# Optimization experiments

Measured on AMD Instinct MI355X. Metric: run time of the kernel, lower is better.

Reference implementation:

```python
import jax, jax.numpy as jnp
import numpy as np

N, D, d = 4_000_000, 3, 2

def setup_inputs() -> dict:
    key = jax.random.key(0)
    k1, k2, k3 = jax.random.split(key, 3)
    points = jax.random.normal(k1, (N, D), dtype=jnp.float32)
    reconstructed_points = jax.random.normal(k2, (N, D), dtype=jnp.float32)
    orthonormal_frame = jax.random.normal(k3, (N, D, d), dtype=jnp.float32)
    return {"points": points, "reconstructed_points": reconstructed_points,
            "orthonormal_frame": orthonormal_frame}

def reference(points, reconstructed_points, orthonormal_frame):
    # r: [N, D] residual
    r = reconstructed_points - points
    # project r onto the tangent frame: y = H @ (H^T r), H: [N, D, d]
    coeffs = jnp.einsum('nij,ni->nj', orthonormal_frame, r)   # [N, d]
    y = jnp.einsum('nij,nj->ni', orthonormal_frame, coeffs)   # [N, D]
    # mean squared norm of the normal component
    diff = r - y
    return jnp.mean(jnp.sum(diff * diff, axis=1))
```

## Files before the change

kernel.cpp:

```cpp
#include <hip/hip_runtime.h>
#include <stdint.h>


#define THREADS 256
#define NWAVES  (THREADS / 64)
#define BLOCKS  768
#define WAVE_LDS 12288

__device__ __forceinline__ void gload_lds16(const void* g, void* l) {
    __builtin_amdgcn_global_load_lds(
        (const __attribute__((address_space(1))) unsigned int*)g,
        (__attribute__((address_space(3))) unsigned int*)l, 16, 0, 0);
}

__global__ __launch_bounds__(THREADS) void ncrl_partial(
    const float* __restrict__ pts,
    const float* __restrict__ rec,
    const float* __restrict__ frame,
    float* __restrict__ partial,
    int nSlices)
{
    __shared__ char stage[WAVE_LDS * NWAVES];
    __shared__ float wsum[NWAVES];

    const int lane = threadIdx.x & 63;
    const int wv   = threadIdx.x >> 6;
    char* wbase = stage + wv * WAVE_LDS;
    const float* Lp = (const float*)(wbase);
    const float* Lr = (const float*)(wbase + 3072);
    const float* Lf = (const float*)(wbase + 6144);

    const float4* P4 = (const float4*)pts;
    const float4* R4 = (const float4*)rec;
    const float4* F4 = (const float4*)frame;

    const int gw0      = blockIdx.x * NWAVES + wv;
    const int gwStride = gridDim.x * NWAVES;

    float acc = 0.0f;
    for (int s = gw0; s < nSlices; s += gwStride) {
        asm volatile("s_waitcnt lgkmcnt(0)" ::: "memory");

        const float4* Pg = P4 + (size_t)s * 192 + lane;
        const float4* Rg = R4 + (size_t)s * 192 + lane;
        const float4* Fg = F4 + (size_t)s * 384 + lane;
#pragma unroll
        for (int i = 0; i < 3; ++i) gload_lds16(Pg + i * 64, wbase + i * 1024);
#pragma unroll
        for (int i = 0; i < 3; ++i) gload_lds16(Rg + i * 64, wbase + 3072 + i * 1024);
#pragma unroll
        for (int i = 0; i < 6; ++i) gload_lds16(Fg + i * 64, wbase + 6144 + i * 1024);

        asm volatile("s_waitcnt vmcnt(0)" ::: "memory");

#pragma unroll
        for (int k = 0; k < 4; ++k) {
            const int p = k * 64 + lane;
            const float a0 = Lp[3 * p], a1 = Lp[3 * p + 1], a2 = Lp[3 * p + 2];
            const float b0 = Lr[3 * p], b1 = Lr[3 * p + 1], b2 = Lr[3 * p + 2];
            const float2 h0 = *(const float2*)(Lf + 6 * p);
            const float2 h1 = *(const float2*)(Lf + 6 * p + 2);
            const float2 h2 = *(const float2*)(Lf + 6 * p + 4);

            const float r0 = b0 - a0, r1 = b1 - a1, r2 = b2 - a2;
            const float c0 = h0.x * r0 + h1.x * r1 + h2.x * r2;
            const float c1 = h0.y * r0 + h1.y * r1 + h2.y * r2;
            const float d0 = r0 - (h0.x * c0 + h0.y * c1);
            const float d1 = r1 - (h1.x * c0 + h1.y * c1);
            const float d2 = r2 - (h2.x * c0 + h2.y * c1);
            acc += d0 * d0 + d1 * d1 + d2 * d2;
        }
    }

#pragma unroll
    for (int off = 32; off > 0; off >>= 1)
        acc += __shfl_down(acc, off, 64);

    if (lane == 0) wsum[wv] = acc;
    __syncthreads();
    if (threadIdx.x == 0) {
        float ssum = 0.0f;
#pragma unroll
        for (int w = 0; w < NWAVES; ++w) ssum += wsum[w];
        partial[blockIdx.x] = ssum;
    }
}

__global__ __launch_bounds__(THREADS) void ncrl_finalize(
    const float* __restrict__ partial,
    const float* __restrict__ pts,
    const float* __restrict__ rec,
    const float* __restrict__ frame,
    float* __restrict__ out,
    int nPartial, int nTailStart, int nPoints)
{
    double acc = 0.0;
    for (int i = threadIdx.x; i < nPartial; i += THREADS)
        acc += (double)partial[i];

    if (threadIdx.x == 0) {
        for (int n = nTailStart; n < nPoints; ++n) {
            const float r0 = rec[3 * n + 0] - pts[3 * n + 0];
            const float r1 = rec[3 * n + 1] - pts[3 * n + 1];
            const float r2 = rec[3 * n + 2] - pts[3 * n + 2];
            const float H00 = frame[6 * n + 0], H01 = frame[6 * n + 1];
            const float H10 = frame[6 * n + 2], H11 = frame[6 * n + 3];
            const float H20 = frame[6 * n + 4], H21 = frame[6 * n + 5];
            const float c0 = H00 * r0 + H10 * r1 + H20 * r2;
            const float c1 = H01 * r0 + H11 * r1 + H21 * r2;
            const float d0 = r0 - (H00 * c0 + H01 * c1);
            const float d1 = r1 - (H10 * c0 + H11 * c1);
            const float d2 = r2 - (H20 * c0 + H21 * c1);
            acc += (double)(d0 * d0 + d1 * d1 + d2 * d2);
        }
    }

#pragma unroll
    for (int off = 32; off > 0; off >>= 1)
        acc += __shfl_down(acc, off, 64);

    __shared__ double dsum[NWAVES];
    const int lane = threadIdx.x & 63;
    const int wv   = threadIdx.x >> 6;
    if (lane == 0) dsum[wv] = acc;
    __syncthreads();
    if (threadIdx.x == 0) {
        double total = 0.0;
#pragma unroll
        for (int w = 0; w < NWAVES; ++w) total += dsum[w];
        out[0] = (float)(total / (double)nPoints);
    }
}

extern "C" void kernel_launch(void* const* d_in, const int* in_sizes, int n_in,
                              void* d_out, int out_size, void* d_ws, size_t ws_size,
                              hipStream_t stream) {
    const float* pts   = (const float*)d_in[0];
    const float* rec   = (const float*)d_in[1];
    const float* frame = (const float*)d_in[2];
    float* out = (float*)d_out;

    const int N       = in_sizes[0] / 3;
    const int nSlices = N / 256;
    const int tail    = nSlices * 256;

    float* partial = (float*)d_ws;

    ncrl_partial<<<BLOCKS, THREADS, 0, stream>>>(pts, rec, frame, partial, nSlices);
    ncrl_finalize<<<1, THREADS, 0, stream>>>(partial, pts, rec, frame, out,
                                             BLOCKS, tail, N);
}
```

Baseline: 207.6 us.

## Double-buffer slice loads in registers to overlap global fetch with compute

The direct global-to-LDS loads, which were each followed by a full vmcnt wait, become register loads into two alternating sets of float4 values. The next slice is issued before the current one is staged into LDS and reduced, so each wave keeps loads in flight during compute instead of stalling on memory every iteration. This raises VGPR use (24 float4 buffers plus an occupancy hint) and adds an extra LDS write pass per slice. Empty asm statements keep the prefetched registers live.

After: 226.4 us. 1.09x slower.

```diff
diff --git a/kernel.cpp b/kernel.cpp
--- a/kernel.cpp
+++ b/kernel.cpp
@@ -7,13 +7,30 @@
 #define BLOCKS  768
 #define WAVE_LDS 12288
 
-__device__ __forceinline__ void gload_lds16(const void* g, void* l) {
-    __builtin_amdgcn_global_load_lds(
-        (const __attribute__((address_space(1))) unsigned int*)g,
-        (__attribute__((address_space(3))) unsigned int*)l, 16, 0, 0);
-}
+#define ISSUE(S, p0,p1,p2,q0,q1,q2,f0,f1,f2,f3,f4v,f5) do {                  \
+    const float4* Pg_ = P4 + (size_t)(S) * 192 + lane;                       \
+    const float4* Rg_ = R4 + (size_t)(S) * 192 + lane;                       \
+    const float4* Fg_ = F4 + (size_t)(S) * 384 + lane;                       \
+    p0 = Pg_[0]; p1 = Pg_[64]; p2 = Pg_[128];                                \
+    q0 = Rg_[0]; q1 = Rg_[64]; q2 = Rg_[128];                                \
+    f0 = Fg_[0]; f1 = Fg_[64]; f2 = Fg_[128];                                \
+    f3 = Fg_[192]; f4v = Fg_[256]; f5 = Fg_[320];                            \
+} while (0)
 
-__global__ __launch_bounds__(THREADS) void ncrl_partial(
+#define STAGE(p0,p1,p2,q0,q1,q2,f0,f1,f2,f3,f4v,f5) do {                     \
+    float4* W_ = (float4*)(wbase) + lane;                                    \
+    W_[0*64] = p0; W_[1*64] = p1; W_[2*64]  = p2;                            \
+    W_[3*64] = q0; W_[4*64] = q1; W_[5*64]  = q2;                            \
+    W_[6*64] = f0; W_[7*64] = f1; W_[8*64]  = f2;                            \
+    W_[9*64] = f3; W_[10*64] = f4v; W_[11*64] = f5;                          \
+} while (0)
+
+#define KEEP(p0,p1,p2,q0,q1,q2,f0,f1,f2,f3,f4v,f5)                           \
+    asm volatile("" :: "v"(p0.x), "v"(p1.x), "v"(p2.x), "v"(q0.x),           \
+                       "v"(q1.x), "v"(q2.x), "v"(f0.x), "v"(f1.x),           \
+                       "v"(f2.x), "v"(f3.x), "v"(f4v.x), "v"(f5.x))
+
+__global__ __launch_bounds__(THREADS, 4) void ncrl_partial(
     const float* __restrict__ pts,
     const float* __restrict__ rec,
     const float* __restrict__ frame,
@@ -37,38 +54,54 @@
     const int gw0      = blockIdx.x * NWAVES + wv;
     const int gwStride = gridDim.x * NWAVES;
 
+    float4 A0, A1, A2, A3, A4, A5, A6, A7, A8, A9, A10, A11;
+    float4 B0, B1, B2, B3, B4, B5, B6, B7, B8, B9, B10, B11;
+
     float acc = 0.0f;
-    for (int s = gw0; s < nSlices; s += gwStride) {
-        asm volatile("s_waitcnt lgkmcnt(0)" ::: "memory");
 
-        const float4* Pg = P4 + (size_t)s * 192 + lane;
-        const float4* Rg = R4 + (size_t)s * 192 + lane;
-        const float4* Fg = F4 + (size_t)s * 384 + lane;
-#pragma unroll
-        for (int i = 0; i < 3; ++i) gload_lds16(Pg + i * 64, wbase + i * 1024);
-#pragma unroll
-        for (int i = 0; i < 3; ++i) gload_lds16(Rg + i * 64, wbase + 3072 + i * 1024);
-#pragma unroll
-        for (int i = 0; i < 6; ++i) gload_lds16(Fg + i * 64, wbase + 6144 + i * 1024);
+#define COMPUTE() do {                                                        \
+    _Pragma("unroll")                                                         \
+    for (int k = 0; k < 4; ++k) {                                             \
+        const int p = k * 64 + lane;                                          \
+        const float a0 = Lp[3*p], a1 = Lp[3*p+1], a2 = Lp[3*p+2];             \
+        const float b0 = Lr[3*p], b1 = Lr[3*p+1], b2 = Lr[3*p+2];             \
+        const float2 h0 = *(const float2*)(Lf + 6*p);                         \
+        const float2 h1 = *(const float2*)(Lf + 6*p + 2);                     \
+        const float2 h2 = *(const float2*)(Lf + 6*p + 4);                     \
+        const float r0 = b0 - a0, r1 = b1 - a1, r2 = b2 - a2;                 \
+        const float c0 = h0.x*r0 + h1.x*r1 + h2.x*r2;                         \
+        const float c1 = h0.y*r0 + h1.y*r1 + h2.y*r2;                         \
+        const float d0 = r0 - (h0.x*c0 + h0.y*c1);                            \
+        const float d1 = r1 - (h1.x*c0 + h1.y*c1);                            \
+        const float d2 = r2 - (h2.x*c0 + h2.y*c1);                            \
+        acc += d0*d0 + d1*d1 + d2*d2;                                         \
+    }                                                                         \
+} while (0)
 
-        asm volatile("s_waitcnt vmcnt(0)" ::: "memory");
+    int s = gw0;
+    if (s < nSlices)
+        ISSUE(s, A0,A1,A2,A3,A4,A5,A6,A7,A8,A9,A10,A11);
 
-#pragma unroll
-        for (int k = 0; k < 4; ++k) {
-            const int p = k * 64 + lane;
-            const float a0 = Lp[3 * p], a1 = Lp[3 * p + 1], a2 = Lp[3 * p + 2];
-            const float b0 = Lr[3 * p], b1 = Lr[3 * p + 1], b2 = Lr[3 * p + 2];
-            const float2 h0 = *(const float2*)(Lf + 6 * p);
-            const float2 h1 = *(const float2*)(Lf + 6 * p + 2);
-            const float2 h2 = *(const float2*)(Lf + 6 * p + 4);
-
-            const float r0 = b0 - a0, r1 = b1 - a1, r2 = b2 - a2;
-            const float c0 = h0.x * r0 + h1.x * r1 + h2.x * r2;
-            const float c1 = h0.y * r0 + h1.y * r1 + h2.y * r2;
-            const float d0 = r0 - (h0.x * c0 + h0.y * c1);
-            const float d1 = r1 - (h1.x * c0 + h1.y * c1);
-            const float d2 = r2 - (h2.x * c0 + h2.y * c1);
-            acc += d0 * d0 + d1 * d1 + d2 * d2;
+    while (s < nSlices) {
+        {
+            const int snext = s + gwStride;
+            if (snext < nSlices)
+                ISSUE(snext, B0,B1,B2,B3,B4,B5,B6,B7,B8,B9,B10,B11);
+            STAGE(A0,A1,A2,A3,A4,A5,A6,A7,A8,A9,A10,A11);
+            COMPUTE();
+            s = snext;
+            if (s >= nSlices) break;
+            KEEP(B0,B1,B2,B3,B4,B5,B6,B7,B8,B9,B10,B11);
+        }
+        {
+            const int snext = s + gwStride;
+            if (snext < nSlices)
+                ISSUE(snext, A0,A1,A2,A3,A4,A5,A6,A7,A8,A9,A10,A11);
+            STAGE(B0,B1,B2,B3,B4,B5,B6,B7,B8,B9,B10,B11);
+            COMPUTE();
+            s = snext;
+            if (s >= nSlices) break;
+            KEEP(A0,A1,A2,A3,A4,A5,A6,A7,A8,A9,A10,A11);
         }
     }
 
@@ -100,18 +133,18 @@
 
     if (threadIdx.x == 0) {
         for (int n = nTailStart; n < nPoints; ++n) {
-            const float r0 = rec[3 * n + 0] - pts[3 * n + 0];
-            const float r1 = rec[3 * n + 1] - pts[3 * n + 1];
-            const float r2 = rec[3 * n + 2] - pts[3 * n + 2];
-            const float H00 = frame[6 * n + 0], H01 = frame[6 * n + 1];
-            const float H10 = frame[6 * n + 2], H11 = frame[6 * n + 3];
-            const float H20 = frame[6 * n + 4], H21 = frame[6 * n + 5];
-            const float c0 = H00 * r0 + H10 * r1 + H20 * r2;
-            const float c1 = H01 * r0 + H11 * r1 + H21 * r2;
-            const float d0 = r0 - (H00 * c0 + H01 * c1);
-            const float d1 = r1 - (H10 * c0 + H11 * c1);
-            const float d2 = r2 - (H20 * c0 + H21 * c1);
-            acc += (double)(d0 * d0 + d1 * d1 + d2 * d2);
+            const float r0 = rec[3*n+0] - pts[3*n+0];
+            const float r1 = rec[3*n+1] - pts[3*n+1];
+            const float r2 = rec[3*n+2] - pts[3*n+2];
+            const float H00 = frame[6*n+0], H01 = frame[6*n+1];
+            const float H10 = frame[6*n+2], H11 = frame[6*n+3];
+            const float H20 = frame[6*n+4], H21 = frame[6*n+5];
+            const float c0 = H00*r0 + H10*r1 + H20*r2;
+            const float c1 = H01*r0 + H11*r1 + H21*r2;
+            const float d0 = r0 - (H00*c0 + H01*c1);
+            const float d1 = r1 - (H10*c0 + H11*c1);
+            const float d2 = r2 - (H20*c0 + H21*c1);
+            acc += (double)(d0*d0 + d1*d1 + d2*d2);
         }
     }
 
```
